# Kernel tuning notes

Hardware: AMD Instinct MI355X
Metric: run time of the kernel (lower is better)

## Reference

```python
import jax, jax.numpy as jnp
import numpy as np

GROUP_SIZE = 128
INTERMEDIATE = 18944


def _unpack_int4(packed):
    # packed: [rows, cols//8] int32, 8 nibbles per int32 along output dim
    shifts = jnp.arange(8, dtype=jnp.int32) * 4
    nib = (packed[:, :, None] >> shifts) & 15  # [rows, cols//8, 8]
    return nib.reshape(packed.shape[0], packed.shape[1] * 8)


def awq_gemm(x, qweight, qzeros, scales, group_size):
    # Dequantize: W[i,j] = (w4[i,j] - z4[i//g, j]) * scales[i//g, j]
    w = _unpack_int4(qweight).astype(jnp.float32)           # [in, out]
    z = _unpack_int4(qzeros).astype(jnp.float32)            # [in//g, out]
    s = scales.astype(jnp.float32)                          # [in//g, out]
    W = ((w - jnp.repeat(z, group_size, axis=0)) * jnp.repeat(s, group_size, axis=0))
    return (x @ W.astype(x.dtype))                          # [tokens, out]


def setup_inputs() -> dict:
    key = jax.random.key(0)
    ks = jax.random.split(key, 7)
    imax = 2147483647
    return {
        "x": (jax.random.normal(ks[0], (4096, 3584), dtype=jnp.float32) * 0.02).astype(jnp.float16),
        "qweight_gu": jax.random.randint(ks[1], (3584, 4736), 0, imax, dtype=jnp.int32),
        "qzeros_gu": jax.random.randint(ks[2], (28, 4736), 0, imax, dtype=jnp.int32),
        "scales_gu": (jax.random.uniform(ks[3], (28, 37888), dtype=jnp.float32) * 0.01 + 0.001).astype(jnp.float16),
        "qweight_down": jax.random.randint(ks[4], (18944, 448), 0, imax, dtype=jnp.int32),
        "qzeros_down": jax.random.randint(ks[5], (148, 448), 0, imax, dtype=jnp.int32),
        "scales_down": (jax.random.uniform(ks[6], (148, 3584), dtype=jnp.float32) * 0.01 + 0.001).astype(jnp.float16),
    }


def reference(x, qweight_gu, qzeros_gu, scales_gu, qweight_down, qzeros_down, scales_down):
    # Fused gate+up AWQ GEMM (matches forward path after fuse_gate_up())
    gate_up = awq_gemm(x, qweight_gu, qzeros_gu, scales_gu, GROUP_SIZE)  # [T, 2*I]
    gate = gate_up[..., :INTERMEDIATE]
    up = gate_up[..., INTERMEDIATE:]
    intermediate = jax.nn.silu(gate) * up                                # fused SiLU*mul
    down = awq_gemm(intermediate, qweight_down, qzeros_down, scales_down, GROUP_SIZE)
    return down
```

## Files before the change

### kernel.cpp

```cpp
#include <hip/hip_runtime.h>
#include <hip/hip_fp16.h>
#include <stdint.h>

typedef _Float16 half8 __attribute__((ext_vector_type(8)));
typedef _Float16 h2v __attribute__((ext_vector_type(2)));
typedef float f32x4 __attribute__((ext_vector_type(4)));

#define GLD_LDS16(gp, lp)                                                     \
  __builtin_amdgcn_global_load_lds(                                           \
      (const __attribute__((address_space(1))) void*)(gp),                    \
      (__attribute__((address_space(3))) void*)(lp), 16, 0, 0)
#define GLD_LDS4(gp, lp)                                                      \
  __builtin_amdgcn_global_load_lds(                                           \
      (const __attribute__((address_space(1))) void*)(gp),                    \
      (__attribute__((address_space(3))) void*)(lp), 4, 0, 0)

__global__ void xcvt_kernel(const float* __restrict__ in, __half* __restrict__ out) {
  const size_t i = ((size_t)blockIdx.x * 256 + threadIdx.x) * 4;
  float4 v = *(const float4*)(in + i);
  __half2* o = (__half2*)(out + i);
  o[0] = __floats2half2_rn(v.x, v.y);
  o[1] = __floats2half2_rn(v.z, v.w);
}

__global__ void repack_kernel(const int* __restrict__ qw, uint32_t* __restrict__ rp, int P) {
  const int N = P * 8;
  const int n = blockIdx.x * 256 + threadIdx.x;
  const int j8 = n >> 3;
  const int sh = (n & 7) * 4;
  #pragma unroll
  for (int qi = 0; qi < 4; ++qi) {
    const int q = blockIdx.y * 4 + qi;
    const int* src = qw + (size_t)(q * 8) * P + j8;
    uint32_t r = 0;
    #pragma unroll
    for (int t = 0; t < 8; ++t) {
      uint32_t w = ((uint32_t)src[t * P] >> sh) & 15u;
      r |= w << (4 * (t >> 1) + 16 * (t & 1));
    }
    rp[(size_t)q * N + n] = r;
  }
}

__global__ void smz_kernel(const float* __restrict__ sc, const int* __restrict__ qz,
                           uint32_t* __restrict__ smz, int P) {
  const int N = P * 8;
  const int n = blockIdx.x * 256 + threadIdx.x;
  const int g = blockIdx.y;
  uint32_t sbits = __half_as_ushort(__float2half(sc[(size_t)g * N + n]));
  uint32_t z = ((uint32_t)qz[(size_t)g * P + (n >> 3)] >> ((n & 7) * 4)) & 15u;
  uint32_t hz = 0x6400u | z;
  smz[(size_t)g * N + n] = sbits | (hz << 16);
}

union U32H2 { uint32_t u; h2v h; };
__device__ inline h2v bith2(uint32_t u) { U32H2 t; t.u = u; return t.h; }
__device__ inline half8 dequant8(uint32_t p, h2v s, h2v z) {
  U32H2 t0, t1, t2, t3;
  t0.u = (p & 0x000F000Fu) | 0x64006400u;
  t1.u = ((p >> 4) & 0x000F000Fu) | 0x64006400u;
  t2.u = ((p >> 8) & 0x000F000Fu) | 0x64006400u;
  t3.u = ((p >> 12) & 0x000F000Fu) | 0x64006400u;
  h2v v0 = (t0.h - z) * s;
  h2v v1 = (t1.h - z) * s;
  h2v v2 = (t2.h - z) * s;
  h2v v3 = (t3.h - z) * s;
  half8 r = {v0.x, v0.y, v1.x, v1.y, v2.x, v2.y, v3.x, v3.y};
  return r;
}

template <int KDIM, int NW, int T1OFF, int OW, bool SILU, int NT, int BXS>
__global__ __launch_bounds__(256, 2) void awq_gemm(const __half* __restrict__ A,
                                                   const uint32_t* __restrict__ RP,
                                                   const uint32_t* __restrict__ SMZ,
                                                   void* __restrict__ OUT) {
  constexpr int ABUF = 128 * 64 * 2;
  constexpr int BBUF = NT * 8 * 128 * 4;
  constexpr int BOFF = 3 * ABUF;
  constexpr int ZOFF = BOFF + 3 * BBUF;
  __shared__ __align__(16) unsigned char smem[ZOFF + 2048];

  const int tid = threadIdx.x;
  const int l = tid & 63;
  const int wv = tid >> 6;
  const int l15 = l & 15;
  const int l4 = l >> 4;

  const int row0 = blockIdx.y * 128;
  const int n0 = blockIdx.x * BXS;

  const __half* asrc[4];
  #pragma unroll
  for (int it = 0; it < 4; ++it) {
    int m = it * 32 + (tid >> 3);
    int cs = tid & 7;
    int kc = cs ^ (m & 7);
    asrc[it] = A + (size_t)(row0 + m) * KDIM + kc * 8;
  }

  const uint32_t* bsrc[NT];
  #pragma unroll
  for (int it = 0; it < NT; ++it) {
    int idx = it * 256 + tid;
    int tile = idx >> 8;
    int qr = (idx >> 5) & 7;
    int l32 = idx & 31;
    int S = ((qr & 1) << 4) | ((qr >> 1) << 2);
    bsrc[it] = RP + (size_t)qr * NW + n0 + tile * T1OFF + ((l32 * 4) ^ S);
  }

  const uint32_t* zsrc = SMZ + n0 + (size_t)(tid >> 7) * T1OFF + (tid & 127);

  f32x4 acc[NT][2][8];
  const f32x4 zero4 = {0.f, 0.f, 0.f, 0.f};
  #pragma unroll
  for (int t = 0; t < NT; ++t)
    #pragma unroll
    for (int nf = 0; nf < 2; ++nf)
      #pragma unroll
      for (int mf = 0; mf < 8; ++mf) acc[t][nf][mf] = zero4;

  uint32_t s2[NT][2], z2[NT][2];
  constexpr int NSTEP = KDIM / 64;

  #pragma unroll
  for (int it = 0; it < 4; ++it)
    GLD_LDS16(asrc[it], &smem[it * 4096 + tid * 16]);
  #pragma unroll
  for (int it = 0; it < NT; ++it)
    GLD_LDS16(bsrc[it], &smem[BOFF + (it * 256 + tid) * 16]);
  GLD_LDS4(zsrc, &smem[ZOFF + tid * 4]);
  #pragma unroll
  for (int it = 0; it < 4; ++it)
    GLD_LDS16(asrc[it] + 64, &smem[ABUF + it * 4096 + tid * 16]);
  #pragma unroll
  for (int it = 0; it < NT; ++it)
    GLD_LDS16(bsrc[it] + (size_t)8 * NW, &smem[BOFF + BBUF + (it * 256 + tid) * 16]);

  int cur = 0, stg = 2;
  for (int t = 0; t < NSTEP; ++t) {
    if (t == NSTEP - 1)      asm volatile("s_waitcnt vmcnt(0)" ::: "memory");
    else if (t & 1)          asm volatile("s_waitcnt vmcnt(7)" ::: "memory");
    else                     asm volatile("s_waitcnt vmcnt(6)" ::: "memory");
    __builtin_amdgcn_s_barrier();

    if (t + 2 < NSTEP) {
      #pragma unroll
      for (int it = 0; it < 4; ++it)
        GLD_LDS16(asrc[it] + (size_t)(t + 2) * 64, &smem[stg * ABUF + it * 4096 + tid * 16]);
      #pragma unroll
      for (int it = 0; it < NT; ++it)
        GLD_LDS16(bsrc[it] + (size_t)(t + 2) * 8 * NW,
                  &smem[BOFF + stg * BBUF + (it * 256 + tid) * 16]);
      if (((t + 2) & 1) == 0) {
        const int g = (t + 2) >> 1;
        GLD_LDS4(zsrc + (size_t)g * NW, &smem[ZOFF + (g & 1) * 1024 + tid * 4]);
      }
    }

    if ((t & 1) == 0) {
      const uint32_t* zl = (const uint32_t*)&smem[ZOFF + ((t >> 1) & 1) * 1024];
      #pragma unroll
      for (int tile = 0; tile < NT; ++tile)
        #pragma unroll
        for (int nf = 0; nf < 2; ++nf) {
          uint32_t u = zl[tile * 128 + wv * 32 + nf * 16 + l15];
          uint32_t lo = u & 0xFFFFu;
          s2[tile][nf] = lo | (lo << 16);
          z2[tile][nf] = (u & 0xFFFF0000u) | (u >> 16);
        }
    }

    uint32_t bq[2][NT][2];
    const int bro = wv * 32 + l15;
    const unsigned char* bbase = &smem[BOFF + cur * BBUF];
    #pragma unroll
    for (int kk = 0; kk < 2; ++kk) {
      const int Sl = ((l4 & 1) << 4) | (kk << 3) | ((l4 >> 1) << 2);
      #pragma unroll
      for (int tile = 0; tile < NT; ++tile)
        #pragma unroll
        for (int nf = 0; nf < 2; ++nf)
          bq[kk][tile][nf] = *(const uint32_t*)&bbase[
              (((tile * 8 + kk * 4 + l4) * 128) + ((bro + nf * 16) ^ Sl)) * 4];
    }

    const unsigned char* abase = &smem[cur * ABUF];
    #pragma unroll
    for (int kk = 0; kk < 2; ++kk) {
      half8 a[8];
      #pragma unroll
      for (int mf = 0; mf < 8; ++mf) {
        int m = mf * 16 + l15;
        int chunk = (kk * 4 + l4) ^ (l15 & 7);
        a[mf] = *(const half8*)(abase + m * 128 + chunk * 16);
      }
      #pragma unroll
      for (int tile = 0; tile < NT; ++tile)
        #pragma unroll
        for (int nf = 0; nf < 2; ++nf) {
          half8 b = dequant8(bq[kk][tile][nf], bith2(s2[tile][nf]), bith2(z2[tile][nf]));
          #pragma unroll
          for (int mf = 0; mf < 8; ++mf)
            acc[tile][nf][mf] =
                __builtin_amdgcn_mfma_f32_16x16x32_f16(a[mf], b, acc[tile][nf][mf], 0, 0, 0);
        }
    }

    cur = (cur == 2) ? 0 : cur + 1;
    stg = (stg == 2) ? 0 : stg + 1;
  }

  if (SILU) {
    __half* O = (__half*)OUT;
    #pragma unroll
    for (int nf = 0; nf < 2; ++nf)
      #pragma unroll
      for (int mf = 0; mf < 8; ++mf)
        #pragma unroll
        for (int r = 0; r < 4; ++r) {
          int row = row0 + mf * 16 + l4 * 4 + r;
          int col = n0 + wv * 32 + nf * 16 + l15;
          float gf = __half2float(__float2half(acc[0][nf][mf][r]));
          float uf = __half2float(__float2half(acc[1][nf][mf][r]));
          float sig = 1.f / (1.f + __expf(-gf));
          float sil = __half2float(__float2half(gf * sig));
          O[(size_t)row * OW + col] = __float2half(sil * uf);
        }
  } else {
    float* O = (float*)OUT;
    #pragma unroll
    for (int tile = 0; tile < NT; ++tile)
      #pragma unroll
      for (int nf = 0; nf < 2; ++nf)
        #pragma unroll
        for (int mf = 0; mf < 8; ++mf)
          #pragma unroll
          for (int r = 0; r < 4; ++r) {
            int row = row0 + mf * 16 + l4 * 4 + r;
            int col = n0 + tile * T1OFF + wv * 32 + nf * 16 + l15;
            O[(size_t)row * OW + col] = __half2float(__float2half(acc[tile][nf][mf][r]));
          }
  }
}

extern "C" void kernel_launch(void* const* d_in, const int* in_sizes, int n_in,
                              void* d_out, int out_size, void* d_ws, size_t ws_size,
                              hipStream_t stream) {
  const float* x_f32 = (const float*)d_in[0];
  const int* qw_gu = (const int*)d_in[1];
  const int* qz_gu = (const int*)d_in[2];
  const float* sc_gu = (const float*)d_in[3];
  const int* qw_dn = (const int*)d_in[4];
  const int* qz_dn = (const int*)d_in[5];
  const float* sc_dn = (const float*)d_in[6];

  char* ws = (char*)d_ws;
  __half* interm   = (__half*)ws;
  uint32_t* rp_gu  = (uint32_t*)(ws + 155189248ull);
  uint32_t* smz_gu = (uint32_t*)(ws + 223084544ull);
  __half* xh       = (__half*)(ws + 227328000ull);
  uint32_t* rp_dn  = (uint32_t*)(ws + 155189248ull);
  uint32_t* smz_dn = (uint32_t*)(ws + 189136896ull);

  xcvt_kernel<<<14336, 256, 0, stream>>>(x_f32, xh);
  repack_kernel<<<dim3(148, 112), 256, 0, stream>>>(qw_gu, rp_gu, 4736);
  smz_kernel<<<dim3(148, 28), 256, 0, stream>>>(sc_gu, qz_gu, smz_gu, 4736);

  awq_gemm<3584, 37888, 18944, 18944, true, 2, 128>
      <<<dim3(148, 32), 256, 0, stream>>>(xh, rp_gu, smz_gu, (void*)interm);

  repack_kernel<<<dim3(14, 592), 256, 0, stream>>>(qw_dn, rp_dn, 448);
  smz_kernel<<<dim3(14, 148), 256, 0, stream>>>(sc_dn, qz_dn, smz_dn, 448);

  awq_gemm<18944, 3584, 128, 3584, false, 2, 256>
      <<<dim3(14, 32), 256, 0, stream>>>(interm, rp_dn, smz_dn, d_out);
}
```

Measured before the change: 1.624 ms.

## Repack weights per column and use a 2x2 wave tiling in AWQ GEMM

```diff
diff --git a/kernel.cpp b/kernel.cpp
--- a/kernel.cpp
+++ b/kernel.cpp
@@ -5,6 +5,7 @@
 typedef _Float16 half8 __attribute__((ext_vector_type(8)));
 typedef _Float16 h2v __attribute__((ext_vector_type(2)));
 typedef float f32x4 __attribute__((ext_vector_type(4)));
+typedef unsigned int u32x2 __attribute__((ext_vector_type(2)));
 
 #define GLD_LDS16(gp, lp)                                                     \
   __builtin_amdgcn_global_load_lds(                                           \
@@ -25,21 +26,22 @@
 
 __global__ void repack_kernel(const int* __restrict__ qw, uint32_t* __restrict__ rp, int P) {
   const int N = P * 8;
-  const int n = blockIdx.x * 256 + threadIdx.x;
-  const int j8 = n >> 3;
-  const int sh = (n & 7) * 4;
-  #pragma unroll
-  for (int qi = 0; qi < 4; ++qi) {
-    const int q = blockIdx.y * 4 + qi;
-    const int* src = qw + (size_t)(q * 8) * P + j8;
-    uint32_t r = 0;
-    #pragma unroll
-    for (int t = 0; t < 8; ++t) {
-      uint32_t w = ((uint32_t)src[t * P] >> sh) & 15u;
-      r |= w << (4 * (t >> 1) + 16 * (t & 1));
-    }
-    rp[(size_t)q * N + n] = r;
-  }
+  const int t = blockIdx.y;
+  const int col = blockIdx.x * 32 + (threadIdx.x >> 3);
+  const int pp = (threadIdx.x >> 1) & 3;
+  const int d = threadIdx.x & 1;
+  const int p = pp ^ ((col >> 2) & 3);
+  const int q = t * 8 + p + 4 * d;
+  const int j8 = col >> 3;
+  const int sh = (col & 7) * 4;
+  const int* src = qw + (size_t)(q * 8) * P + j8;
+  uint32_t r = 0;
+  #pragma unroll
+  for (int tt = 0; tt < 8; ++tt) {
+    uint32_t w = ((uint32_t)src[tt * P] >> sh) & 15u;
+    r |= w << (4 * (tt >> 1) + 16 * (tt & 1));
+  }
+  rp[((size_t)t * N + col) * 8 + pp * 2 + d] = r;
 }
 
 __global__ void smz_kernel(const float* __restrict__ sc, const int* __restrict__ qz,
@@ -69,13 +71,13 @@
   return r;
 }
 
-template <int KDIM, int NW, int T1OFF, int OW, bool SILU, int NT, int BXS>
+template <int KDIM, int NW, int T1OFF, int OW, bool SILU, int BXS>
 __global__ __launch_bounds__(256, 2) void awq_gemm(const __half* __restrict__ A,
                                                    const uint32_t* __restrict__ RP,
                                                    const uint32_t* __restrict__ SMZ,
                                                    void* __restrict__ OUT) {
   constexpr int ABUF = 128 * 64 * 2;
-  constexpr int BBUF = NT * 8 * 128 * 4;
+  constexpr int BBUF = 2 * 1024 * 4;
   constexpr int BOFF = 3 * ABUF;
   constexpr int ZOFF = BOFF + 3 * BBUF;
   __shared__ __align__(16) unsigned char smem[ZOFF + 2048];
@@ -83,6 +85,8 @@
   const int tid = threadIdx.x;
   const int l = tid & 63;
   const int wv = tid >> 6;
+  const int h = wv >> 1;
+  const int q = wv & 1;
   const int l15 = l & 15;
   const int l4 = l >> 4;
 
@@ -98,44 +102,43 @@
     asrc[it] = A + (size_t)(row0 + m) * KDIM + kc * 8;
   }
 
-  const uint32_t* bsrc[NT];
-  #pragma unroll
-  for (int it = 0; it < NT; ++it) {
-    int idx = it * 256 + tid;
-    int tile = idx >> 8;
-    int qr = (idx >> 5) & 7;
-    int l32 = idx & 31;
-    int S = ((qr & 1) << 4) | ((qr >> 1) << 2);
-    bsrc[it] = RP + (size_t)qr * NW + n0 + tile * T1OFF + ((l32 * 4) ^ S);
-  }
+  const uint32_t* bsrc[2];
+  #pragma unroll
+  for (int tl = 0; tl < 2; ++tl)
+    bsrc[tl] = RP + ((size_t)(n0 + tl * T1OFF)) * 8 + tid * 4;
 
   const uint32_t* zsrc = SMZ + n0 + (size_t)(tid >> 7) * T1OFF + (tid & 127);
 
-  f32x4 acc[NT][2][8];
+  f32x4 acc[2][4][4];
   const f32x4 zero4 = {0.f, 0.f, 0.f, 0.f};
   #pragma unroll
-  for (int t = 0; t < NT; ++t)
-    #pragma unroll
-    for (int nf = 0; nf < 2; ++nf)
-      #pragma unroll
-      for (int mf = 0; mf < 8; ++mf) acc[t][nf][mf] = zero4;
-
-  uint32_t s2[NT][2], z2[NT][2];
+  for (int tl = 0; tl < 2; ++tl)
+    #pragma unroll
+    for (int fi = 0; fi < 4; ++fi)
+      #pragma unroll
+      for (int mf = 0; mf < 4; ++mf) acc[tl][fi][mf] = zero4;
+
+  uint32_t s2[2][4], z2[2][4];
   constexpr int NSTEP = KDIM / 64;
+
+  const int aoff0 = (h * 64 + l15) * 128 + ((0 * 4 + l4) ^ (l15 & 7)) * 16;
+  const int aoff1 = (h * 64 + l15) * 128 + ((1 * 4 + l4) ^ (l15 & 7)) * 16;
+  const int boff = (q * 64 + l15) * 32 + (l4 ^ ((l15 >> 2) & 3)) * 8;
+  const int zidx = q * 64 + l15;
 
   #pragma unroll
   for (int it = 0; it < 4; ++it)
     GLD_LDS16(asrc[it], &smem[it * 4096 + tid * 16]);
   #pragma unroll
-  for (int it = 0; it < NT; ++it)
-    GLD_LDS16(bsrc[it], &smem[BOFF + (it * 256 + tid) * 16]);
+  for (int tl = 0; tl < 2; ++tl)
+    GLD_LDS16(bsrc[tl], &smem[BOFF + tl * 4096 + tid * 16]);
   GLD_LDS4(zsrc, &smem[ZOFF + tid * 4]);
   #pragma unroll
   for (int it = 0; it < 4; ++it)
     GLD_LDS16(asrc[it] + 64, &smem[ABUF + it * 4096 + tid * 16]);
   #pragma unroll
-  for (int it = 0; it < NT; ++it)
-    GLD_LDS16(bsrc[it] + (size_t)8 * NW, &smem[BOFF + BBUF + (it * 256 + tid) * 16]);
+  for (int tl = 0; tl < 2; ++tl)
+    GLD_LDS16(bsrc[tl] + (size_t)NW * 8, &smem[BOFF + BBUF + tl * 4096 + tid * 16]);
 
   int cur = 0, stg = 2;
   for (int t = 0; t < NSTEP; ++t) {
@@ -149,9 +152,9 @@
       for (int it = 0; it < 4; ++it)
         GLD_LDS16(asrc[it] + (size_t)(t + 2) * 64, &smem[stg * ABUF + it * 4096 + tid * 16]);
       #pragma unroll
-      for (int it = 0; it < NT; ++it)
-        GLD_LDS16(bsrc[it] + (size_t)(t + 2) * 8 * NW,
-                  &smem[BOFF + stg * BBUF + (it * 256 + tid) * 16]);
+      for (int tl = 0; tl < 2; ++tl)
+        GLD_LDS16(bsrc[tl] + (size_t)(t + 2) * NW * 8,
+                  &smem[BOFF + stg * BBUF + tl * 4096 + tid * 16]);
       if (((t + 2) & 1) == 0) {
         const int g = (t + 2) >> 1;
         GLD_LDS4(zsrc + (size_t)g * NW, &smem[ZOFF + (g & 1) * 1024 + tid * 4]);
@@ -161,49 +164,42 @@
     if ((t & 1) == 0) {
       const uint32_t* zl = (const uint32_t*)&smem[ZOFF + ((t >> 1) & 1) * 1024];
       #pragma unroll
-      for (int tile = 0; tile < NT; ++tile)
-        #pragma unroll
-        for (int nf = 0; nf < 2; ++nf) {
-          uint32_t u = zl[tile * 128 + wv * 32 + nf * 16 + l15];
+      for (int tl = 0; tl < 2; ++tl)
+        #pragma unroll
+        for (int fi = 0; fi < 4; ++fi) {
+          uint32_t u = zl[tl * 128 + fi * 16 + zidx];
           uint32_t lo = u & 0xFFFFu;
-          s2[tile][nf] = lo | (lo << 16);
-          z2[tile][nf] = (u & 0xFFFF0000u) | (u >> 16);
+          s2[tl][fi] = lo | (lo << 16);
+          z2[tl][fi] = (u & 0xFFFF0000u) | (u >> 16);
         }
     }
 
-    uint32_t bq[2][NT][2];
-    const int bro = wv * 32 + l15;
+    u32x2 bq[2][4];
     const unsigned char* bbase = &smem[BOFF + cur * BBUF];
     #pragma unroll
+    for (int tl = 0; tl < 2; ++tl)
+      #pragma unroll
+      for (int fi = 0; fi < 4; ++fi)
+        bq[tl][fi] = *(const u32x2*)&bbase[boff + tl * 4096 + fi * 512];
+
+    const unsigned char* abase = &smem[cur * ABUF];
+    #pragma unroll
     for (int kk = 0; kk < 2; ++kk) {
-      const int Sl = ((l4 & 1) << 4) | (kk << 3) | ((l4 >> 1) << 2);
-      #pragma unroll
-      for (int tile = 0; tile < NT; ++tile)
-        #pragma unroll
-        for (int nf = 0; nf < 2; ++nf)
-          bq[kk][tile][nf] = *(const uint32_t*)&bbase[
-              (((tile * 8 + kk * 4 + l4) * 128) + ((bro + nf * 16) ^ Sl)) * 4];
-    }
-
-    const unsigned char* abase = &smem[cur * ABUF];
-    #pragma unroll
-    for (int kk = 0; kk < 2; ++kk) {
-      half8 a[8];
-      #pragma unroll
-      for (int mf = 0; mf < 8; ++mf) {
-        int m = mf * 16 + l15;
-        int chunk = (kk * 4 + l4) ^ (l15 & 7);
-        a[mf] = *(const half8*)(abase + m * 128 + chunk * 16);
-      }
-      #pragma unroll
-      for (int tile = 0; tile < NT; ++tile)
-        #pragma unroll
-        for (int nf = 0; nf < 2; ++nf) {
-          half8 b = dequant8(bq[kk][tile][nf], bith2(s2[tile][nf]), bith2(z2[tile][nf]));
+      half8 a[4];
+      const int ao = kk ? aoff1 : aoff0;
+      #pragma unroll
+      for (int mf = 0; mf < 4; ++mf)
+        a[mf] = *(const half8*)(abase + ao + mf * 2048);
+      #pragma unroll
+      for (int tl = 0; tl < 2; ++tl)
+        #pragma unroll
+        for (int fi = 0; fi < 4; ++fi) {
+          half8 b = dequant8(kk ? bq[tl][fi].y : bq[tl][fi].x,
+                             bith2(s2[tl][fi]), bith2(z2[tl][fi]));
           #pragma unroll
-          for (int mf = 0; mf < 8; ++mf)
-            acc[tile][nf][mf] =
-                __builtin_amdgcn_mfma_f32_16x16x32_f16(a[mf], b, acc[tile][nf][mf], 0, 0, 0);
+          for (int mf = 0; mf < 4; ++mf)
+            acc[tl][fi][mf] =
+                __builtin_amdgcn_mfma_f32_16x16x32_f16(a[mf], b, acc[tl][fi][mf], 0, 0, 0);
         }
     }
 
@@ -214,15 +210,15 @@
   if (SILU) {
     __half* O = (__half*)OUT;
     #pragma unroll
-    for (int nf = 0; nf < 2; ++nf)
-      #pragma unroll
-      for (int mf = 0; mf < 8; ++mf)
+    for (int fi = 0; fi < 4; ++fi)
+      #pragma unroll
+      for (int mf = 0; mf < 4; ++mf)
         #pragma unroll
         for (int r = 0; r < 4; ++r) {
-          int row = row0 + mf * 16 + l4 * 4 + r;
-          int col = n0 + wv * 32 + nf * 16 + l15;
-          float gf = __half2float(__float2half(acc[0][nf][mf][r]));
-          float uf = __half2float(__float2half(acc[1][nf][mf][r]));
+          int row = row0 + h * 64 + mf * 16 + l4 * 4 + r;
+          int col = n0 + q * 64 + fi * 16 + l15;
+          float gf = __half2float(__float2half(acc[0][fi][mf][r]));
+          float uf = __half2float(__float2half(acc[1][fi][mf][r]));
           float sig = 1.f / (1.f + __expf(-gf));
           float sil = __half2float(__float2half(gf * sig));
           O[(size_t)row * OW + col] = __float2half(sil * uf);
@@ -230,16 +226,16 @@
   } else {
     float* O = (float*)OUT;
     #pragma unroll
-    for (int tile = 0; tile < NT; ++tile)
-      #pragma unroll
-      for (int nf = 0; nf < 2; ++nf)
-        #pragma unroll
-        for (int mf = 0; mf < 8; ++mf)
+    for (int tl = 0; tl < 2; ++tl)
+      #pragma unroll
+      for (int fi = 0; fi < 4; ++fi)
+        #pragma unroll
+        for (int mf = 0; mf < 4; ++mf)
           #pragma unroll
           for (int r = 0; r < 4; ++r) {
-            int row = row0 + mf * 16 + l4 * 4 + r;
-            int col = n0 + tile * T1OFF + wv * 32 + nf * 16 + l15;
-            O[(size_t)row * OW + col] = __half2float(__float2half(acc[tile][nf][mf][r]));
+            int row = row0 + h * 64 + mf * 16 + l4 * 4 + r;
+            int col = n0 + tl * T1OFF + q * 64 + fi * 16 + l15;
+            O[(size_t)row * OW + col] = __half2float(__float2half(acc[tl][fi][mf][r]));
           }
   }
 }
@@ -264,15 +260,15 @@
   uint32_t* smz_dn = (uint32_t*)(ws + 189136896ull);
 
   xcvt_kernel<<<14336, 256, 0, stream>>>(x_f32, xh);
-  repack_kernel<<<dim3(148, 112), 256, 0, stream>>>(qw_gu, rp_gu, 4736);
+  repack_kernel<<<dim3(1184, 56), 256, 0, stream>>>(qw_gu, rp_gu, 4736);
   smz_kernel<<<dim3(148, 28), 256, 0, stream>>>(sc_gu, qz_gu, smz_gu, 4736);
 
-  awq_gemm<3584, 37888, 18944, 18944, true, 2, 128>
+  awq_gemm<3584, 37888, 18944, 18944, true, 128>
       <<<dim3(148, 32), 256, 0, stream>>>(xh, rp_gu, smz_gu, (void*)interm);
 
-  repack_kernel<<<dim3(14, 592), 256, 0, stream>>>(qw_dn, rp_dn, 448);
+  repack_kernel<<<dim3(112, 296), 256, 0, stream>>>(qw_dn, rp_dn, 448);
   smz_kernel<<<dim3(14, 148), 256, 0, stream>>>(sc_dn, qz_dn, smz_dn, 448);
 
-  awq_gemm<18944, 3584, 128, 3584, false, 2, 256>
+  awq_gemm<18944, 3584, 128, 3584, false, 256>
       <<<dim3(14, 32), 256, 0, stream>>>(interm, rp_dn, smz_dn, d_out);
 }
```

New measurement: 1.982 ms. 22.1% more time.
